# Kernel tuning notes

Hardware: AMD Instinct MI355X
Metric: run time of the kernel (lower is better)

## Reference

```python
import jax, jax.numpy as jnp
import numpy as np

# cv2.getGaussianKernel(5, 0) returns the fixed small-kernel table [1,4,6,4,1]/16
_K5 = jnp.array([1.0, 4.0, 6.0, 4.0, 1.0], dtype=jnp.float32) / 16.0


def _blur5(x):
    """Separable 5x5 Gaussian blur with BORDER_REFLECT_101 (cv2 default). x: (..., H, W)."""
    H, W = x.shape[-2], x.shape[-1]
    pad = [(0, 0)] * (x.ndim - 2) + [(2, 2), (2, 2)]
    xp = jnp.pad(x, pad, mode='reflect')  # reflect == REFLECT_101
    xh = sum(_K5[i] * xp[..., i:i + H, :] for i in range(5))      # conv along H
    return sum(_K5[j] * xh[..., :, j:j + W] for j in range(5))    # conv along W


def _erode(m):
    # skimage binary_erosion: cross footprint, out-of-image treated as True
    p = [(0, 0)] * (m.ndim - 2) + [(1, 1), (1, 1)]
    mp = jnp.pad(m, p, constant_values=True)
    return (mp[..., 1:-1, 1:-1] & mp[..., :-2, 1:-1] & mp[..., 2:, 1:-1]
            & mp[..., 1:-1, :-2] & mp[..., 1:-1, 2:])


def _dilate(m):
    # skimage binary_dilation: cross footprint, out-of-image treated as False
    p = [(0, 0)] * (m.ndim - 2) + [(1, 1), (1, 1)]
    mp = jnp.pad(m, p, constant_values=False)
    return (mp[..., 1:-1, 1:-1] | mp[..., :-2, 1:-1] | mp[..., 2:, 1:-1]
            | mp[..., 1:-1, :-2] | mp[..., 1:-1, 2:])


def _fill_holes(m):
    """remove_small_holes with area_threshold > H*W == fill every enclosed hole.
    Background = flood fill of ~m seeded from the image border (4-connectivity)."""
    comp = ~m
    H, W = m.shape[-2], m.shape[-1]
    border = jnp.zeros((H, W), bool)
    border = border.at[0, :].set(True).at[-1, :].set(True)
    border = border.at[:, 0].set(True).at[:, -1].set(True)
    seed = comp & border

    def cond(st):
        return st[1]

    def body(st):
        s, _ = st
        ns = comp & _dilate(s)
        return ns, jnp.any(ns != s)

    bg, _ = jax.lax.while_loop(cond, body, (seed, jnp.array(True)))
    return ~bg  # foreground plus all enclosed holes


def _get_mask(img, maxv, th):
    """clip -> uint8 quantize -> 5x5 Gaussian blur -> threshold -> opening -> hole fill."""
    norm = jnp.clip(img, 0.0, maxv) / maxv            # min_=0, max_=img.max()
    q = jnp.floor(255.0 * norm)                        # np.uint8 cast truncates
    b = jnp.round(_blur5(q))                           # cv2 uint8 blur rounds to nearest
    m = b > th
    m = _dilate(_erode(m))                             # binary opening, cross footprint
    return _fill_holes(m)


def setup_inputs() -> dict:
    key = jax.random.key(0)
    x = jax.random.normal(key, (16, 37, 224, 224), dtype=jnp.float32)
    return {"input": x, "label": 1}


def reference(input, label):
    if label:
        lab = jnp.argmax(input, axis=1).astype(jnp.float32)            # (B, H, W)
        maxv = lab.max(axis=(-2, -1), keepdims=True)
        m = _get_mask(lab, maxv, 0.0)
        out = jnp.repeat(m[:, None], 3, axis=1)                        # (B, 3, H, W)
    else:
        x = (input + 1.0) / 2.0
        maxv = x.max(axis=(-3, -2, -1), keepdims=True)
        m = _get_mask(x, maxv, 55.0)
        out = m
    return out.astype(jnp.float32)
```

## Files before the change

### kernel.cpp

```cpp
#include <hip/hip_runtime.h>
#include <stdint.h>

#define NB 16
#define NC 37
#define H 224
#define W 224
#define HW (H * W)
#define WPR 7
#define IMG_WORDS (H * WPR)
#define QUADS_PER_IMG (HW / 4)
#define BLOCKS_PER_IMG (QUADS_PER_IMG / 256)
#define REPS 16
#define OUT_Q4_PER_IMG (3 * H * (W / 4))
#define OUT_Q4_PER_REP (OUT_Q4_PER_IMG / REPS)

__global__ __launch_bounds__(256) void k_argmax(const float* __restrict__ in,
                                                uint8_t* __restrict__ lab,
                                                int* __restrict__ bmax) {
    const int b = blockIdx.x / BLOCKS_PER_IMG;
    const int qid = blockIdx.x * 256 + threadIdx.x;
    const int p = (qid % QUADS_PER_IMG) * 4;
    const float4* base = (const float4*)(in + (size_t)b * NC * HW + p);
    float4 bv = base[0];
    int ix = 0, iy = 0, iz = 0, iw = 0;
#pragma unroll
    for (int c = 1; c < NC; c += 4) {
        float4 a0 = base[(size_t)(c + 0) * (HW / 4)];
        float4 a1 = base[(size_t)(c + 1) * (HW / 4)];
        float4 a2 = base[(size_t)(c + 2) * (HW / 4)];
        float4 a3 = base[(size_t)(c + 3) * (HW / 4)];
        if (a0.x > bv.x) { bv.x = a0.x; ix = c; }
        if (a0.y > bv.y) { bv.y = a0.y; iy = c; }
        if (a0.z > bv.z) { bv.z = a0.z; iz = c; }
        if (a0.w > bv.w) { bv.w = a0.w; iw = c; }
        if (a1.x > bv.x) { bv.x = a1.x; ix = c + 1; }
        if (a1.y > bv.y) { bv.y = a1.y; iy = c + 1; }
        if (a1.z > bv.z) { bv.z = a1.z; iz = c + 1; }
        if (a1.w > bv.w) { bv.w = a1.w; iw = c + 1; }
        if (a2.x > bv.x) { bv.x = a2.x; ix = c + 2; }
        if (a2.y > bv.y) { bv.y = a2.y; iy = c + 2; }
        if (a2.z > bv.z) { bv.z = a2.z; iz = c + 2; }
        if (a2.w > bv.w) { bv.w = a2.w; iw = c + 2; }
        if (a3.x > bv.x) { bv.x = a3.x; ix = c + 3; }
        if (a3.y > bv.y) { bv.y = a3.y; iy = c + 3; }
        if (a3.z > bv.z) { bv.z = a3.z; iz = c + 3; }
        if (a3.w > bv.w) { bv.w = a3.w; iw = c + 3; }
    }
    uint32_t packed = (uint32_t)ix | ((uint32_t)iy << 8) |
                      ((uint32_t)iz << 16) | ((uint32_t)iw << 24);
    *(uint32_t*)(lab + (size_t)b * HW + p) = packed;

    int mymax = max(max(ix, iy), max(iz, iw));
    __shared__ int smax;
    if (threadIdx.x == 0) smax = 0;
    __syncthreads();
    atomicMax(&smax, mymax);
    __syncthreads();
    if (threadIdx.x == 0) bmax[blockIdx.x] = smax;
}

__global__ __launch_bounds__(256) void k_mask(const uint8_t* __restrict__ lab,
                                              const int* __restrict__ bmax,
                                              uint32_t* __restrict__ mbits) {
    __shared__ int qlut[NC];
    __shared__ int smax;
    const int tid = threadIdx.x;
    const int b = blockIdx.x / BLOCKS_PER_IMG;
    if (tid == 0) smax = 0;
    __syncthreads();
    if (tid < BLOCKS_PER_IMG) atomicMax(&smax, bmax[b * BLOCKS_PER_IMG + tid]);
    __syncthreads();
    if (tid < NC) {
        int mv = smax;
        qlut[tid] = (mv > 0) ? (int)floorf(255.0f * ((float)tid / (float)mv)) : 0;
    }
    __syncthreads();

    const int qid = blockIdx.x * 256 + tid;
    const int rem = qid % QUADS_PER_IMG;
    const int h = rem / (W / 4);
    const int w0 = (rem % (W / 4)) * 4;
    const uint8_t* __restrict__ L = lab + (size_t)b * HW;

    int S0 = 0, S1 = 0, S2 = 0, S3 = 0;
    const int kw5[5] = {1, 4, 6, 4, 1};
#pragma unroll
    for (int i = 0; i < 5; ++i) {
        int r = h + i - 2;
        r = (r < 0) ? -r : ((r > H - 1) ? (2 * (H - 1) - r) : r);
        const uint8_t* row = L + r * W;
        int q0, q1, q2, q3, q4, q5, q6, q7;
        if (w0 >= 4 && w0 <= W - 8) {
            uint32_t wa = *(const uint32_t*)(row + w0 - 4);
            uint32_t wb = *(const uint32_t*)(row + w0);
            uint32_t wc = *(const uint32_t*)(row + w0 + 4);
            q0 = qlut[(wa >> 16) & 0xff];
            q1 = qlut[(wa >> 24) & 0xff];
            q2 = qlut[wb & 0xff];
            q3 = qlut[(wb >> 8) & 0xff];
            q4 = qlut[(wb >> 16) & 0xff];
            q5 = qlut[(wb >> 24) & 0xff];
            q6 = qlut[wc & 0xff];
            q7 = qlut[(wc >> 8) & 0xff];
        } else {
            int qq[8];
#pragma unroll
            for (int t = 0; t < 8; ++t) {
                int c2 = w0 - 2 + t;
                c2 = (c2 < 0) ? -c2 : ((c2 > W - 1) ? (2 * (W - 1) - c2) : c2);
                qq[t] = qlut[row[c2]];
            }
            q0 = qq[0]; q1 = qq[1]; q2 = qq[2]; q3 = qq[3];
            q4 = qq[4]; q5 = qq[5]; q6 = qq[6]; q7 = qq[7];
        }
        int sh0 = q0 + 4 * q1 + 6 * q2 + 4 * q3 + q4;
        int sh1 = q1 + 4 * q2 + 6 * q3 + 4 * q4 + q5;
        int sh2 = q2 + 4 * q3 + 6 * q4 + 4 * q5 + q6;
        int sh3 = q3 + 4 * q4 + 6 * q5 + 4 * q6 + q7;
        int k = kw5[i];
        S0 += k * sh0; S1 += k * sh1; S2 += k * sh2; S3 += k * sh3;
    }
    uint32_t nib = (S0 > 128 ? 1u : 0u) | (S1 > 128 ? 2u : 0u) |
                   (S2 > 128 ? 4u : 0u) | (S3 > 128 ? 8u : 0u);
    uint32_t wword = nib << ((tid & 7) * 4);
    wword |= __shfl_xor(wword, 1);
    wword |= __shfl_xor(wword, 2);
    wword |= __shfl_xor(wword, 4);
    if ((tid & 7) == 0) mbits[qid >> 3] = wword;
}

__global__ __launch_bounds__(256) void k_fillexp(const uint32_t* __restrict__ mbits,
                                                 float* __restrict__ out) {
    const int img = blockIdx.x >> 4;
    const int rep = blockIdx.x & 15;
    const int tid = threadIdx.x;
    __shared__ uint32_t A[IMG_WORDS];
    __shared__ uint32_t Bw[IMG_WORDS];
    __shared__ int s_changed;

    const uint32_t* src = mbits + img * IMG_WORDS;
    for (int i = tid; i < IMG_WORDS; i += 256) A[i] = src[i];
    __syncthreads();

    for (int i = tid; i < IMG_WORDS; i += 256) {
        int h = i / WPR, k = i % WPR;
        uint32_t cur = A[i];
        uint32_t north = (h > 0) ? A[i - WPR] : 0xFFFFFFFFu;
        uint32_t south = (h < H - 1) ? A[i + WPR] : 0xFFFFFFFFu;
        uint32_t west = (cur << 1) | ((k > 0) ? (A[i - 1] >> 31) : 1u);
        uint32_t east = (cur >> 1) | ((k < WPR - 1) ? (A[i + 1] << 31) : 0x80000000u);
        Bw[i] = cur & north & south & west & east;
    }
    __syncthreads();
    for (int i = tid; i < IMG_WORDS; i += 256) {
        int h = i / WPR, k = i % WPR;
        uint32_t cur = Bw[i];
        uint32_t north = (h > 0) ? Bw[i - WPR] : 0u;
        uint32_t south = (h < H - 1) ? Bw[i + WPR] : 0u;
        uint32_t west = (cur << 1) | ((k > 0) ? (Bw[i - 1] >> 31) : 0u);
        uint32_t east = (cur >> 1) | ((k < WPR - 1) ? (Bw[i + 1] << 31) : 0u);
        A[i] = cur | north | south | west | east;
    }
    __syncthreads();
    for (int i = tid; i < IMG_WORDS; i += 256) {
        int h = i / WPR, k = i % WPR;
        uint32_t comp = ~A[i];
        uint32_t border = (h == 0 || h == H - 1)
                              ? 0xFFFFFFFFu
                              : (((k == 0) ? 1u : 0u) | ((k == WPR - 1) ? 0x80000000u : 0u));
        Bw[i] = comp & border;
    }
    __syncthreads();

    while (true) {
        if (tid == 0) s_changed = 0;
        __syncthreads();
        if (tid < WPR) {
            const int k = tid;
            uint32_t carry = 0;
            for (int h = 0; h < H; ++h) {
                int i = h * WPR + k;
                uint32_t comp = ~A[i];
                uint32_t s = Bw[i];
                uint32_t ns = comp & (s | carry);
                if (ns != s) { Bw[i] = ns; s_changed = 1; }
                carry = ns;
            }
            carry = 0;
            for (int h = H - 1; h >= 0; --h) {
                int i = h * WPR + k;
                uint32_t comp = ~A[i];
                uint32_t s = Bw[i];
                uint32_t ns = comp & (s | carry);
                if (ns != s) { Bw[i] = ns; s_changed = 1; }
                carry = ns;
            }
        }
        __syncthreads();
        if (tid < H) {
            const int base = tid * WPR;
            uint32_t carry = 0;
            for (int k = 0; k < WPR; ++k) {
                uint32_t comp = ~A[base + k];
                uint32_t s = Bw[base + k];
                if (comp == 0u) { carry = 0u; continue; }
                uint32_t f = s | (carry & comp);
                uint32_t m = comp;
                f |= m & (f << 1);  m &= (m << 1);
                f |= m & (f << 2);  m &= (m << 2);
                f |= m & (f << 4);  m &= (m << 4);
                f |= m & (f << 8);  m &= (m << 8);
                f |= m & (f << 16);
                carry = f >> 31;
                if (f != s) { Bw[base + k] = f; s_changed = 1; }
            }
            carry = 0;
            for (int k = WPR - 1; k >= 0; --k) {
                uint32_t comp = ~A[base + k];
                uint32_t s = Bw[base + k];
                if (comp == 0u) { carry = 0u; continue; }
                uint32_t f = s | ((carry << 31) & comp);
                uint32_t m = comp;
                f |= m & (f >> 1);  m &= (m >> 1);
                f |= m & (f >> 2);  m &= (m >> 2);
                f |= m & (f >> 4);  m &= (m >> 4);
                f |= m & (f >> 8);  m &= (m >> 8);
                f |= m & (f >> 16);
                carry = f & 1u;
                if (f != s) { Bw[base + k] = f; s_changed = 1; }
            }
        }
        __syncthreads();
        int done = (s_changed == 0);
        __syncthreads();
        if (done) break;
    }

    float4* outq = (float4*)out + (size_t)img * OUT_Q4_PER_IMG;
    for (int oi = rep * OUT_Q4_PER_REP + tid; oi < (rep + 1) * OUT_Q4_PER_REP;
         oi += 256) {
        int remq = oi % QUADS_PER_IMG;
        int h = remq / (W / 4);
        int wq = remq % (W / 4);
        uint32_t word = ~Bw[h * WPR + (wq >> 3)];
        int sh = (wq & 7) * 4;
        float4 v;
        v.x = ((word >> sh) & 1u) ? 1.0f : 0.0f;
        v.y = ((word >> (sh + 1)) & 1u) ? 1.0f : 0.0f;
        v.z = ((word >> (sh + 2)) & 1u) ? 1.0f : 0.0f;
        v.w = ((word >> (sh + 3)) & 1u) ? 1.0f : 0.0f;
        outq[oi] = v;
    }
}

extern "C" void kernel_launch(void* const* d_in, const int* in_sizes, int n_in,
                              void* d_out, int out_size, void* d_ws, size_t ws_size,
                              hipStream_t stream) {
    const float* in = (const float*)d_in[0];
    float* out = (float*)d_out;

    uint8_t* lab = (uint8_t*)d_ws;
    int* bmax = (int*)((char*)d_ws + 802816);
    uint32_t* mbits = (uint32_t*)((char*)d_ws + 806400);

    k_argmax<<<NB * BLOCKS_PER_IMG, 256, 0, stream>>>(in, lab, bmax);
    k_mask<<<NB * BLOCKS_PER_IMG, 256, 0, stream>>>(lab, bmax, mbits);
    k_fillexp<<<NB * REPS, 256, 0, stream>>>(mbits, out);
}
```

Before: 215.1 us.

## Parallelize vertical flood-fill sweep via bit-matrix transpose in shared memory

Replaces the vertical flood-fill pass, which ran serially over 224 rows on only 7 threads, with a 32x32 bit-matrix transpose done with wave shuffles. The same bit-parallel horizontal smear can then run on 224 threads over the transposed columns, after which the result is transposed back. Each iteration now pays for two transposes, extra shared memory (two more image-sized arrays) and the removal of the skip-when-solid shortcut, in exchange for far more parallelism in the column direction.

```diff
diff --git a/kernel.cpp b/kernel.cpp
--- a/kernel.cpp
+++ b/kernel.cpp
@@ -129,6 +129,75 @@
     if ((tid & 7) == 0) mbits[qid >> 3] = wword;
 }
 
+__device__ __forceinline__ void bit_transpose(const uint32_t* __restrict__ src,
+                                              uint32_t* __restrict__ dst,
+                                              int tid) {
+    const int wave = tid >> 6;
+    const int half = (tid >> 5) & 1;
+    const int lane5 = tid & 31;
+    const uint32_t M1 = 0x55555555u, M2 = 0x33333333u, M4 = 0x0F0F0F0Fu,
+                   M8 = 0x00FF00FFu, M16 = 0x0000FFFFu;
+#pragma unroll
+    for (int t0 = 0; t0 < 49; t0 += 8) {
+        int t = t0 + wave * 2 + half;
+        if (t < 49) {
+            int I = t / 7, J = t % 7;
+            uint32_t v = src[(32 * I + lane5) * WPR + J];
+            uint32_t o;
+            o = __shfl_xor(v, 1);
+            v = (lane5 & 1) ? ((v & ~M1) | ((o >> 1) & M1)) : ((v & M1) | ((o & M1) << 1));
+            o = __shfl_xor(v, 2);
+            v = (lane5 & 2) ? ((v & ~M2) | ((o >> 2) & M2)) : ((v & M2) | ((o & M2) << 2));
+            o = __shfl_xor(v, 4);
+            v = (lane5 & 4) ? ((v & ~M4) | ((o >> 4) & M4)) : ((v & M4) | ((o & M4) << 4));
+            o = __shfl_xor(v, 8);
+            v = (lane5 & 8) ? ((v & ~M8) | ((o >> 8) & M8)) : ((v & M8) | ((o & M8) << 8));
+            o = __shfl_xor(v, 16);
+            v = (lane5 & 16) ? ((v & ~M16) | ((o >> 16) & M16)) : ((v & M16) | ((o & M16) << 16));
+            dst[(32 * J + lane5) * WPR + I] = v;
+        }
+    }
+}
+
+__device__ __forceinline__ uint32_t ks_smear_line(uint32_t* __restrict__ Bw,
+                                                  const uint32_t* __restrict__ A,
+                                                  int base) {
+    uint32_t chg = 0;
+    uint32_t carry = 0;
+#pragma unroll
+    for (int k = 0; k < WPR; ++k) {
+        uint32_t comp = ~A[base + k];
+        uint32_t s = Bw[base + k];
+        uint32_t f = s | (carry & comp);
+        uint32_t m = comp;
+        f |= m & (f << 1);  m &= (m << 1);
+        f |= m & (f << 2);  m &= (m << 2);
+        f |= m & (f << 4);  m &= (m << 4);
+        f |= m & (f << 8);  m &= (m << 8);
+        f |= m & (f << 16);
+        carry = f >> 31;
+        chg |= f ^ s;
+        Bw[base + k] = f;
+    }
+    carry = 0;
+#pragma unroll
+    for (int k = WPR - 1; k >= 0; --k) {
+        uint32_t comp = ~A[base + k];
+        uint32_t s = Bw[base + k];
+        uint32_t f = s | ((carry << 31) & comp);
+        uint32_t m = comp;
+        f |= m & (f >> 1);  m &= (m >> 1);
+        f |= m & (f >> 2);  m &= (m >> 2);
+        f |= m & (f >> 4);  m &= (m >> 4);
+        f |= m & (f >> 8);  m &= (m >> 8);
+        f |= m & (f >> 16);
+        carry = f & 1u;
+        chg |= f ^ s;
+        Bw[base + k] = f;
+    }
+    return chg;
+}
+
 __global__ __launch_bounds__(256) void k_fillexp(const uint32_t* __restrict__ mbits,
                                                  float* __restrict__ out) {
     const int img = blockIdx.x >> 4;
@@ -136,6 +205,8 @@
     const int tid = threadIdx.x;
     __shared__ uint32_t A[IMG_WORDS];
     __shared__ uint32_t Bw[IMG_WORDS];
+    __shared__ uint32_t AT[IMG_WORDS];
+    __shared__ uint32_t BT[IMG_WORDS];
     __shared__ int s_changed;
 
     const uint32_t* src = mbits + img * IMG_WORDS;
@@ -170,70 +241,25 @@
                               : (((k == 0) ? 1u : 0u) | ((k == WPR - 1) ? 0x80000000u : 0u));
         Bw[i] = comp & border;
     }
+    bit_transpose(A, AT, tid);
     __syncthreads();
 
     while (true) {
         if (tid == 0) s_changed = 0;
         __syncthreads();
-        if (tid < WPR) {
-            const int k = tid;
-            uint32_t carry = 0;
-            for (int h = 0; h < H; ++h) {
-                int i = h * WPR + k;
-                uint32_t comp = ~A[i];
-                uint32_t s = Bw[i];
-                uint32_t ns = comp & (s | carry);
-                if (ns != s) { Bw[i] = ns; s_changed = 1; }
-                carry = ns;
-            }
-            carry = 0;
-            for (int h = H - 1; h >= 0; --h) {
-                int i = h * WPR + k;
-                uint32_t comp = ~A[i];
-                uint32_t s = Bw[i];
-                uint32_t ns = comp & (s | carry);
-                if (ns != s) { Bw[i] = ns; s_changed = 1; }
-                carry = ns;
-            }
-        }
-        __syncthreads();
         if (tid < H) {
-            const int base = tid * WPR;
-            uint32_t carry = 0;
-            for (int k = 0; k < WPR; ++k) {
-                uint32_t comp = ~A[base + k];
-                uint32_t s = Bw[base + k];
-                if (comp == 0u) { carry = 0u; continue; }
-                uint32_t f = s | (carry & comp);
-                uint32_t m = comp;
-                f |= m & (f << 1);  m &= (m << 1);
-                f |= m & (f << 2);  m &= (m << 2);
-                f |= m & (f << 4);  m &= (m << 4);
-                f |= m & (f << 8);  m &= (m << 8);
-                f |= m & (f << 16);
-                carry = f >> 31;
-                if (f != s) { Bw[base + k] = f; s_changed = 1; }
-            }
-            carry = 0;
-            for (int k = WPR - 1; k >= 0; --k) {
-                uint32_t comp = ~A[base + k];
-                uint32_t s = Bw[base + k];
-                if (comp == 0u) { carry = 0u; continue; }
-                uint32_t f = s | ((carry << 31) & comp);
-                uint32_t m = comp;
-                f |= m & (f >> 1);  m &= (m >> 1);
-                f |= m & (f >> 2);  m &= (m >> 2);
-                f |= m & (f >> 4);  m &= (m >> 4);
-                f |= m & (f >> 8);  m &= (m >> 8);
-                f |= m & (f >> 16);
-                carry = f & 1u;
-                if (f != s) { Bw[base + k] = f; s_changed = 1; }
-            }
-        }
-        __syncthreads();
-        int done = (s_changed == 0);
-        __syncthreads();
-        if (done) break;
+            if (ks_smear_line(Bw, A, tid * WPR)) s_changed = 1;
+        }
+        __syncthreads();
+        bit_transpose(Bw, BT, tid);
+        __syncthreads();
+        if (tid < W) {
+            if (ks_smear_line(BT, AT, tid * WPR)) s_changed = 1;
+        }
+        __syncthreads();
+        bit_transpose(BT, Bw, tid);
+        __syncthreads();
+        if (!s_changed) break;
     }
 
     float4* outq = (float4*)out + (size_t)img * OUT_Q4_PER_IMG;
```

Result: faster. 199.8 us (-7.1%).
